# Performance work log

Hardware: AMD Instinct MI355X
Metric: run time of the kernel (lower is better)

Reference implementation:

```python
import jax, jax.numpy as jnp
import numpy as np

N_NODES = 100000
N_EDGES = 1600000
D_IN, D_HID, D_OUT = 64, 128, 64


def setup_inputs() -> dict:
    key = jax.random.key(0)
    ks = jax.random.split(key, 12)
    s = lambda d: 1.0 / np.sqrt(d)
    return {
        "x": jax.random.normal(ks[0], (N_NODES, D_IN), dtype=jnp.float32),
        "edge_index": jax.random.randint(ks[1], (2, N_EDGES), 0, N_NODES, dtype=jnp.int64),
        # conv1 MLP: Linear(D_IN->D_HID), ReLU, Linear(D_HID->D_HID)
        "W1a": jax.random.uniform(ks[2], (D_IN, D_HID), jnp.float32, -s(D_IN), s(D_IN)),
        "b1a": jnp.zeros((D_HID,), jnp.float32),
        "W1b": jax.random.uniform(ks[3], (D_HID, D_HID), jnp.float32, -s(D_HID), s(D_HID)),
        "b1b": jnp.zeros((D_HID,), jnp.float32),
        # conv2 MLP: Linear(D_HID->D_HID), ReLU, Linear(D_HID->D_HID)
        "W2a": jax.random.uniform(ks[4], (D_HID, D_HID), jnp.float32, -s(D_HID), s(D_HID)),
        "b2a": jnp.zeros((D_HID,), jnp.float32),
        "W2b": jax.random.uniform(ks[5], (D_HID, D_HID), jnp.float32, -s(D_HID), s(D_HID)),
        "b2b": jnp.zeros((D_HID,), jnp.float32),
        # final projection Linear(D_HID->D_OUT)
        "Wlin": jax.random.uniform(ks[6], (D_HID, D_OUT), jnp.float32, -s(D_HID), s(D_HID)),
        "blin": jnp.zeros((D_OUT,), jnp.float32),
    }


def _gin_conv(h, src, dst, Wa, ba, Wb, bb, num_nodes):
    # GINConv (eps=0): MLP((1+eps)*x + sum_{j->i} x_j)
    agg = jax.ops.segment_sum(h[src], dst, num_segments=num_nodes)  # [N, d]
    z = h + agg
    z = jax.nn.relu(z @ Wa + ba)
    return z @ Wb + bb


def reference(x, edge_index, W1a, b1a, W1b, b1b, W2a, b2a, W2b, b2b, Wlin, blin):
    n = x.shape[0]
    src, dst = edge_index[0], edge_index[1]
    h = jax.nn.relu(_gin_conv(x, src, dst, W1a, b1a, W1b, b1b, n))
    h = jax.nn.relu(_gin_conv(h, src, dst, W2a, b2a, W2b, b2b, n))
    return h @ Wlin + blin  # [N, D_OUT]
```

## Files before the change

kernel.cpp:

```cpp
#include <hip/hip_runtime.h>
#include <hip/hip_fp16.h>


typedef __attribute__((ext_vector_type(8))) short short8;
typedef __attribute__((ext_vector_type(4))) float f32x4;
union F8 { unsigned u[4]; short8 s; };

__device__ inline unsigned bfpair(float v) {
    unsigned u = __float_as_uint(v);
    unsigned rh = u + 0x7fffu + ((u >> 16) & 1u);
    unsigned hf = rh & 0xffff0000u;
    float lof = v - __uint_as_float(hf);
    unsigned ul = __float_as_uint(lof);
    unsigned rl = ul + 0x7fffu + ((ul >> 16) & 1u);
    return (rh >> 16) | (rl & 0xffff0000u);
}


constexpr int BUCKET_SHIFT = 9;
constexpr int BUCKET_NODES = 1 << BUCKET_SHIFT;
constexpr int CAP = 10240;
constexpr int EPB = 4096;
constexpr int NBUCK_MAX = 256;

__global__ __launch_bounds__(256) void bucket_scatter_kernel(const int* __restrict__ ei, int E,
                                                             int* __restrict__ gcur,
                                                             int* __restrict__ gpk,
                                                             int nbuck) {
    __shared__ int spk[EPB];
    __shared__ unsigned char sbuck[EPB];
    __shared__ int lcnt[NBUCK_MAX];
    __shared__ int lbase[NBUCK_MAX];
    __shared__ int lcur[NBUCK_MAX];
    __shared__ int gbase[NBUCK_MAX];
    __shared__ int stmp[256];

    const int t = threadIdx.x;
    const int e0 = blockIdx.x * EPB;
    const int ecnt = min(EPB, E - e0);

    for (int i = t; i < NBUCK_MAX; i += 256) lcnt[i] = 0;
    __syncthreads();

    for (int i = t; i < ecnt; i += 256) {
        int d = ei[E + e0 + i];
        atomicAdd(&lcnt[d >> BUCKET_SHIFT], 1);
    }
    __syncthreads();

    int v = lcnt[t];
    stmp[t] = v;
    __syncthreads();
    #pragma unroll
    for (int off = 1; off < 256; off <<= 1) {
        int add = (t >= off) ? stmp[t - off] : 0;
        __syncthreads();
        stmp[t] += add;
        __syncthreads();
    }
    lbase[t] = stmp[t] - v;
    lcur[t] = stmp[t] - v;
    __syncthreads();

    for (int i = t; i < ecnt; i += 256) {
        int s = ei[e0 + i];
        int d = ei[E + e0 + i];
        int b = d >> BUCKET_SHIFT;
        int p = atomicAdd(&lcur[b], 1);
        spk[p] = ((d & (BUCKET_NODES - 1)) << 17) | s;
        sbuck[p] = (unsigned char)b;
    }
    __syncthreads();

    if (t < nbuck) {
        int c = lcnt[t];
        gbase[t] = (c > 0) ? atomicAdd(&gcur[t], c) : 0;
    }
    __syncthreads();

    for (int i = t; i < ecnt; i += 256) {
        int b = sbuck[i];
        int gp = gbase[b] + (i - lbase[b]);
        if (gp < (b + 1) * CAP) gpk[gp] = spk[i];
    }
}

__global__ __launch_bounds__(256) void bucket_hist_kernel(const int* __restrict__ gpk,
                                                          const int* __restrict__ gcur,
                                                          int* __restrict__ cnt, int N) {
    __shared__ int h[BUCKET_NODES];
    const int t = threadIdx.x;
    const int b = blockIdx.x;
    const int base = b << BUCKET_SHIFT;
    for (int i = t; i < BUCKET_NODES; i += 256) h[i] = 0;
    __syncthreads();
    int cb = min(gcur[b] - b * CAP, CAP);
    const int* pp = gpk + (size_t)b * CAP;
    for (int i = t; i < cb; i += 256) atomicAdd(&h[((unsigned)pp[i]) >> 17], 1);
    __syncthreads();
    for (int i = t; i < BUCKET_NODES && base + i < N; i += 256) cnt[base + i] = h[i];
}

__global__ __launch_bounds__(256) void scan_block_kernel(const int* __restrict__ cnt,
                                                         int* __restrict__ rs,
                                                         int* __restrict__ partials,
                                                         int N) {
    __shared__ int s[256];
    int t = threadIdx.x;
    int i = blockIdx.x * 256 + t;
    int v = (i < N) ? cnt[i] : 0;
    s[t] = v;
    __syncthreads();
    #pragma unroll
    for (int off = 1; off < 256; off <<= 1) {
        int add = (t >= off) ? s[t - off] : 0;
        __syncthreads();
        s[t] += add;
        __syncthreads();
    }
    if (i < N) rs[i] = s[t] - v;
    if (t == 255) partials[blockIdx.x] = s[255];
}

__global__ __launch_bounds__(512) void scan_partials_kernel(int* __restrict__ partials,
                                                            int nb) {
    __shared__ int s[512];
    int t = threadIdx.x;
    int v = (t < nb) ? partials[t] : 0;
    s[t] = v;
    __syncthreads();
    #pragma unroll
    for (int off = 1; off < 512; off <<= 1) {
        int add = (t >= off) ? s[t - off] : 0;
        __syncthreads();
        s[t] += add;
        __syncthreads();
    }
    if (t < nb) partials[t] = s[t] - v;
}

__global__ __launch_bounds__(256) void scan_add_kernel(int* __restrict__ rs,
                                                       const int* __restrict__ partials,
                                                       int N, int E) {
    int i = blockIdx.x * 256 + threadIdx.x;
    if (i < N) rs[i] += partials[blockIdx.x];
    if (i == 0) rs[N] = E;
}

__global__ __launch_bounds__(256) void bucket_fill_kernel(const int* __restrict__ gpk,
                                                          const int* __restrict__ gcur,
                                                          const int* __restrict__ rs,
                                                          int* __restrict__ edge_src, int N) {
    __shared__ int cur[BUCKET_NODES];
    const int t = threadIdx.x;
    const int b = blockIdx.x;
    const int base = b << BUCKET_SHIFT;
    for (int i = t; i < BUCKET_NODES; i += 256) cur[i] = rs[min(base + i, N)];
    __syncthreads();
    int cb = min(gcur[b] - b * CAP, CAP);
    const int* pp = gpk + (size_t)b * CAP;
    for (int i = t; i < cb; i += 256) {
        unsigned pw = (unsigned)pp[i];
        int p = atomicAdd(&cur[pw >> 17], 1);
        edge_src[p] = (int)(pw & 0x1FFFFu);
    }
}


__global__ __launch_bounds__(256) void prep_kernel(const float* __restrict__ W1a,
                                                   const float* __restrict__ W1b,
                                                   const float* __restrict__ W2a,
                                                   const float* __restrict__ W2b,
                                                   const float* __restrict__ Wlin,
                                                   short* __restrict__ hi,
                                                   short* __restrict__ lo,
                                                   const float* __restrict__ x,
                                                   __half2* __restrict__ x16, int n2,
                                                   int* __restrict__ gcur, int nbuck) {
    int i = blockIdx.x * 256 + threadIdx.x;
    if (blockIdx.x == 0 && threadIdx.x < nbuck) gcur[threadIdx.x] = threadIdx.x * CAP;
    if (i < 65536) {
        const float* W;
        int base, K, N;
        if (i < 8192)       { W = W1a;  base = 0;     K = 64;  N = 128; }
        else if (i < 24576) { W = W1b;  base = 8192;  K = 128; N = 128; }
        else if (i < 40960) { W = W2a;  base = 24576; K = 128; N = 128; }
        else if (i < 57344) { W = W2b;  base = 40960; K = 128; N = 128; }
        else                { W = Wlin; base = 57344; K = 128; N = 64;  }
        int rel = i - base;
        int NT = N >> 4;
        int j  = rel & 7;
        int l  = (rel >> 3) & 63;
        int tc = rel >> 9;
        int nt = tc % NT;
        int c  = tc / NT;
        int n  = nt * 16 + (l & 15);
        int k  = c * 32 + ((l >> 4) << 3) + j;
        float v = W[k * N + n];
        unsigned p = bfpair(v);
        hi[i] = (short)(p & 0xffffu);
        lo[i] = (short)(p >> 16);
    }
    for (int k = i; k < n2; k += gridDim.x * 256) {
        float2 v = reinterpret_cast<const float2*>(x)[k];
        x16[k] = __floats2half2_rn(v.x, v.y);
    }
}


__device__ inline void acc8(float* a, const uint4& v) {
    const __half2* h = reinterpret_cast<const __half2*>(&v);
    #pragma unroll
    for (int j = 0; j < 4; ++j) {
        float2 f = __half22float2(h[j]);
        a[2 * j]     += f.x;
        a[2 * j + 1] += f.y;
    }
}

__device__ inline uint4 pack8(const float* a) {
    uint4 o;
    __half2 h;
    h = __floats2half2_rn(a[0], a[1]); o.x = *reinterpret_cast<unsigned*>(&h);
    h = __floats2half2_rn(a[2], a[3]); o.y = *reinterpret_cast<unsigned*>(&h);
    h = __floats2half2_rn(a[4], a[5]); o.z = *reinterpret_cast<unsigned*>(&h);
    h = __floats2half2_rn(a[6], a[7]); o.w = *reinterpret_cast<unsigned*>(&h);
    return o;
}

__global__ __launch_bounds__(256) void agg128_fp16(const __half2* __restrict__ H16,
                                                   const int* __restrict__ row_start,
                                                   const int* __restrict__ edge_src,
                                                   __half2* __restrict__ Z16, int N) {
    int wave = threadIdx.x >> 6, lane = threadIdx.x & 63;
    int node = blockIdx.x * 4 + wave;
    if (node >= N) return;
    const int lg = lane >> 4;
    const int lo = lane & 15;
    const uint4* Hv = reinterpret_cast<const uint4*>(H16);
    int beg = row_start[node], end = row_start[node + 1];

    uint4 selfv = Hv[(size_t)node * 16 + lo];

    float a[8];
    #pragma unroll
    for (int j = 0; j < 8; ++j) a[j] = 0.f;
    if (lg == 0) acc8(a, selfv);

    int i = beg;
    for (; i + 16 <= end; i += 16) {
        int s0 = edge_src[i + lg];
        int s1 = edge_src[i + 4 + lg];
        int s2 = edge_src[i + 8 + lg];
        int s3 = edge_src[i + 12 + lg];
        uint4 v0 = Hv[(size_t)s0 * 16 + lo];
        uint4 v1 = Hv[(size_t)s1 * 16 + lo];
        uint4 v2 = Hv[(size_t)s2 * 16 + lo];
        uint4 v3 = Hv[(size_t)s3 * 16 + lo];
        acc8(a, v0); acc8(a, v1); acc8(a, v2); acc8(a, v3);
    }
    if (i + 8 <= end) {
        int s0 = edge_src[i + lg];
        int s1 = edge_src[i + 4 + lg];
        uint4 v0 = Hv[(size_t)s0 * 16 + lo];
        uint4 v1 = Hv[(size_t)s1 * 16 + lo];
        acc8(a, v0); acc8(a, v1);
        i += 8;
    }
    if (i + 4 <= end) {
        int s0 = edge_src[i + lg];
        uint4 v0 = Hv[(size_t)s0 * 16 + lo];
        acc8(a, v0);
        i += 4;
    }
    int rem = end - i;
    if (lg < rem) {
        int s0 = edge_src[i + lg];
        uint4 v0 = Hv[(size_t)s0 * 16 + lo];
        acc8(a, v0);
    }

    #pragma unroll
    for (int j = 0; j < 8; ++j) {
        a[j] += __shfl_xor(a[j], 16);
        a[j] += __shfl_xor(a[j], 32);
    }

    if (lg == 0) {
        reinterpret_cast<uint4*>(Z16)[(size_t)node * 16 + lo] = pack8(a);
    }
}

__global__ __launch_bounds__(256) void agg64_fp16(const __half2* __restrict__ H16,
                                                  const int* __restrict__ row_start,
                                                  const int* __restrict__ edge_src,
                                                  __half2* __restrict__ Z16, int N) {
    int wave = threadIdx.x >> 6, lane = threadIdx.x & 63;
    int node = blockIdx.x * 4 + wave;
    if (node >= N) return;
    const int lg = lane >> 3;
    const int lo = lane & 7;
    const uint4* Hv = reinterpret_cast<const uint4*>(H16);
    int beg = row_start[node], end = row_start[node + 1];

    uint4 selfv = Hv[(size_t)node * 8 + lo];

    float a[8];
    #pragma unroll
    for (int j = 0; j < 8; ++j) a[j] = 0.f;
    if (lg == 0) acc8(a, selfv);

    int i = beg;
    for (; i + 16 <= end; i += 16) {
        int s0 = edge_src[i + lg];
        int s1 = edge_src[i + 8 + lg];
        uint4 v0 = Hv[(size_t)s0 * 8 + lo];
        uint4 v1 = Hv[(size_t)s1 * 8 + lo];
        acc8(a, v0); acc8(a, v1);
    }
    if (i + 8 <= end) {
        int s0 = edge_src[i + lg];
        uint4 v0 = Hv[(size_t)s0 * 8 + lo];
        acc8(a, v0);
        i += 8;
    }
    int rem = end - i;
    if (lg < rem) {
        int s0 = edge_src[i + lg];
        uint4 v0 = Hv[(size_t)s0 * 8 + lo];
        acc8(a, v0);
    }

    #pragma unroll
    for (int j = 0; j < 8; ++j) {
        a[j] += __shfl_xor(a[j], 8);
        a[j] += __shfl_xor(a[j], 16);
        a[j] += __shfl_xor(a[j], 32);
    }

    if (lg == 0) {
        reinterpret_cast<uint4*>(Z16)[(size_t)node * 8 + lo] = pack8(a);
    }
}


template <int K>
__device__ inline void stage_global16(const __half2* __restrict__ z, int M, int m0,
                                      unsigned* __restrict__ P, int t) {
    constexpr int KC = K / 32;
    constexpr int NF = 8 * KC * 64;
    #pragma unroll
    for (int fi = t; fi < NF; fi += 256) {
        int l = fi & 63;
        int tc = fi >> 6;
        int c = tc & (KC - 1);
        int T = tc / KC;
        int row = m0 + T * 16 + (l & 15);
        if (row >= M) row = M - 1;
        int kb = c * 32 + ((l >> 4) << 3);
        const __half2* p = z + (size_t)row * (K / 2) + (kb >> 1);
        uint4 v = *reinterpret_cast<const uint4*>(p);
        float2 f0 = __half22float2(*reinterpret_cast<__half2*>(&v.x));
        float2 f1 = __half22float2(*reinterpret_cast<__half2*>(&v.y));
        float2 f2 = __half22float2(*reinterpret_cast<__half2*>(&v.z));
        float2 f3 = __half22float2(*reinterpret_cast<__half2*>(&v.w));
        int base = ((T * KC + c) * 8) * 66 + l;
        P[base + 0 * 66] = bfpair(f0.x);
        P[base + 1 * 66] = bfpair(f0.y);
        P[base + 2 * 66] = bfpair(f1.x);
        P[base + 3 * 66] = bfpair(f1.y);
        P[base + 4 * 66] = bfpair(f2.x);
        P[base + 5 * 66] = bfpair(f2.y);
        P[base + 6 * 66] = bfpair(f3.x);
        P[base + 7 * 66] = bfpair(f3.y);
    }
}

template <int K, int NT>
__device__ inline void stage_compute(const unsigned* __restrict__ P,
                                     const short* __restrict__ WH,
                                     const short* __restrict__ WL,
                                     int w, int lane, f32x4 (*acc)[8]) {
    constexpr int KC = K / 32;
    const short8* bhp = reinterpret_cast<const short8*>(WH) + lane;
    const short8* blp = reinterpret_cast<const short8*>(WL) + lane;
    for (int c = 0; c < KC; ++c) {
        F8 bh[NT], bl[NT];
        #pragma unroll
        for (int nt = 0; nt < NT; ++nt) {
            bh[nt].s = bhp[(c * NT + nt) * 64];
            bl[nt].s = blp[(c * NT + nt) * 64];
        }
        #pragma unroll
        for (int mt = 0; mt < 2; ++mt) {
            const int T = w * 2 + mt;
            const unsigned* Pb = P + ((T * KC + c) * 8) * 66 + lane;
            unsigned d[8];
            #pragma unroll
            for (int j = 0; j < 8; ++j) d[j] = Pb[j * 66];
            F8 ah, al;
            #pragma unroll
            for (int j = 0; j < 4; ++j) {
                ah.u[j] = __builtin_amdgcn_perm(d[2 * j + 1], d[2 * j], 0x05040100u);
                al.u[j] = __builtin_amdgcn_perm(d[2 * j + 1], d[2 * j], 0x07060302u);
            }
            #pragma unroll
            for (int nt = 0; nt < NT; ++nt) {
                acc[mt][nt] = __builtin_amdgcn_mfma_f32_16x16x32_bf16(ah.s, bh[nt].s, acc[mt][nt], 0, 0, 0);
                acc[mt][nt] = __builtin_amdgcn_mfma_f32_16x16x32_bf16(al.s, bh[nt].s, acc[mt][nt], 0, 0, 0);
                acc[mt][nt] = __builtin_amdgcn_mfma_f32_16x16x32_bf16(ah.s, bl[nt].s, acc[mt][nt], 0, 0, 0);
            }
        }
    }
}

__device__ inline void epilogue_tile(const f32x4* acc, const float* __restrict__ bias,
                                     unsigned* __restrict__ Pout, int T, int lane) {
    int q = lane >> 4, ln = lane & 15;
    #pragma unroll
    for (int nt = 0; nt < 8; ++nt) {
        int col = nt * 16 + ln;
        float b = bias[col];
        int c = col >> 5, jj = col & 7, q2 = (col >> 3) & 3;
        int pb = ((T * 4 + c) * 8 + jj) * 66;
        #pragma unroll
        for (int r = 0; r < 4; ++r) {
            float v = fmaxf(acc[nt][r] + b, 0.f);
            Pout[pb + ((q * 4 + r) | (q2 << 4))] = bfpair(v);
        }
    }
}

__global__ __launch_bounds__(256, 2) void mfma_mlp_A(const __half2* __restrict__ z16,
                                                     const short* __restrict__ WaH,
                                                     const short* __restrict__ WaL,
                                                     const float* __restrict__ ba,
                                                     const short* __restrict__ WbH,
                                                     const short* __restrict__ WbL,
                                                     const float* __restrict__ bb,
                                                     __half* __restrict__ H16out, int M) {
    __shared__ unsigned P[8 * 4 * 8 * 66];
    const int t = threadIdx.x;
    const int w = t >> 6, lane = t & 63;
    const int m0 = blockIdx.x * 128;
    const int q = lane >> 4, ln = lane & 15;

    stage_global16<64>(z16, M, m0, P, t);
    __syncthreads();

    f32x4 acc[2][8];
    #pragma unroll
    for (int mt = 0; mt < 2; ++mt)
        #pragma unroll
        for (int i = 0; i < 8; ++i) acc[mt][i] = (f32x4){0.f, 0.f, 0.f, 0.f};
    stage_compute<64, 8>(P, WaH, WaL, w, lane, acc);
    __syncthreads();
    epilogue_tile(acc[0], ba, P, w * 2 + 0, lane);
    epilogue_tile(acc[1], ba, P, w * 2 + 1, lane);
    __syncthreads();

    #pragma unroll
    for (int mt = 0; mt < 2; ++mt)
        #pragma unroll
        for (int i = 0; i < 8; ++i) acc[mt][i] = (f32x4){0.f, 0.f, 0.f, 0.f};
    stage_compute<128, 8>(P, WbH, WbL, w, lane, acc);

    #pragma unroll
    for (int mt = 0; mt < 2; ++mt) {
        #pragma unroll
        for (int nt = 0; nt < 8; ++nt) {
            int col = nt * 16 + ln;
            float b = bb[col];
            #pragma unroll
            for (int r = 0; r < 4; ++r) {
                int row = m0 + (w * 2 + mt) * 16 + q * 4 + r;
                if (row < M) {
                    float v = fmaxf(acc[mt][nt][r] + b, 0.f);
                    H16out[(size_t)row * 128 + col] = __float2half_rn(v);
                }
            }
        }
    }
}

__global__ __launch_bounds__(256, 2) void mfma_mlp_B(const __half2* __restrict__ z16,
                                                     const short* __restrict__ WaH,
                                                     const short* __restrict__ WaL,
                                                     const float* __restrict__ ba,
                                                     const short* __restrict__ WbH,
                                                     const short* __restrict__ WbL,
                                                     const float* __restrict__ bb,
                                                     const short* __restrict__ WlH,
                                                     const short* __restrict__ WlL,
                                                     const float* __restrict__ bl,
                                                     float* __restrict__ Out, int M) {
    __shared__ unsigned P[8 * 4 * 8 * 66];
    const int t = threadIdx.x;
    const int w = t >> 6, lane = t & 63;
    const int m0 = blockIdx.x * 128;
    const int q = lane >> 4, ln = lane & 15;

    stage_global16<128>(z16, M, m0, P, t);
    __syncthreads();

    f32x4 acc[2][8];
    #pragma unroll
    for (int mt = 0; mt < 2; ++mt)
        #pragma unroll
        for (int i = 0; i < 8; ++i) acc[mt][i] = (f32x4){0.f, 0.f, 0.f, 0.f};
    stage_compute<128, 8>(P, WaH, WaL, w, lane, acc);
    __syncthreads();
    epilogue_tile(acc[0], ba, P, w * 2 + 0, lane);
    epilogue_tile(acc[1], ba, P, w * 2 + 1, lane);
    __syncthreads();

    #pragma unroll
    for (int mt = 0; mt < 2; ++mt)
        #pragma unroll
        for (int i = 0; i < 8; ++i) acc[mt][i] = (f32x4){0.f, 0.f, 0.f, 0.f};
    stage_compute<128, 8>(P, WbH, WbL, w, lane, acc);
    __syncthreads();
    epilogue_tile(acc[0], bb, P, w * 2 + 0, lane);
    epilogue_tile(acc[1], bb, P, w * 2 + 1, lane);
    __syncthreads();

    #pragma unroll
    for (int mt = 0; mt < 2; ++mt)
        #pragma unroll
        for (int i = 0; i < 8; ++i) acc[mt][i] = (f32x4){0.f, 0.f, 0.f, 0.f};
    stage_compute<128, 4>(P, WlH, WlL, w, lane, acc);

    #pragma unroll
    for (int mt = 0; mt < 2; ++mt) {
        #pragma unroll
        for (int nt = 0; nt < 4; ++nt) {
            int col = nt * 16 + ln;
            float b = bl[col];
            #pragma unroll
            for (int r = 0; r < 4; ++r) {
                int row = m0 + (w * 2 + mt) * 16 + q * 4 + r;
                if (row < M) Out[(size_t)row * 64 + col] = acc[mt][nt][r] + b;
            }
        }
    }
}


extern "C" void kernel_launch(void* const* d_in, const int* in_sizes, int n_in,
                              void* d_out, int out_size, void* d_ws, size_t ws_size,
                              hipStream_t stream) {
    const float* x    = (const float*)d_in[0];
    const int*   ei   = (const int*)d_in[1];
    const float* W1a  = (const float*)d_in[2];
    const float* b1a  = (const float*)d_in[3];
    const float* W1b  = (const float*)d_in[4];
    const float* b1b  = (const float*)d_in[5];
    const float* W2a  = (const float*)d_in[6];
    const float* b2a  = (const float*)d_in[7];
    const float* W2b  = (const float*)d_in[8];
    const float* b2b  = (const float*)d_in[9];
    const float* Wlin = (const float*)d_in[10];
    const float* blin = (const float*)d_in[11];
    float* out = (float*)d_out;

    const int N = in_sizes[0] / 64;
    const int E = in_sizes[1] / 2;
    const int NBUCK = (N + BUCKET_NODES - 1) >> BUCKET_SHIFT;

    char* ws = (char*)d_ws;
    const size_t bufBytes = (size_t)N * 128 * sizeof(float);
    __half2* Zbuf = (__half2*)(ws + 0);
    char* B = ws + bufBytes;
    size_t off = 3 * bufBytes;
    int* row_start = (int*)(ws + off); off += ((size_t)(N + 1) * 4 + 15) & ~(size_t)15;
    int* cnt       = (int*)(ws + off); off += ((size_t)N * 4 + 15) & ~(size_t)15;
    int* partials  = (int*)(ws + off); off += 4096;
    int* gcur      = (int*)(ws + off); off += 4096;
    int* edge_src  = (int*)(ws + off); off += (size_t)E * 4;
    __half* h116   = (__half*)(ws + off); off += (size_t)N * 128 * 2;
    int* gpk = (int*)B;
    short* wHi = (short*)(B + (32u << 20));
    short* wLo = wHi + 65536;
    __half* x16 = (__half*)(B + (36u << 20));
    short* w1aH = wHi + 0;     short* w1aL = wLo + 0;
    short* w1bH = wHi + 8192;  short* w1bL = wLo + 8192;
    short* w2aH = wHi + 24576; short* w2aL = wLo + 24576;
    short* w2bH = wHi + 40960; short* w2bL = wLo + 40960;
    short* wlH  = wHi + 57344; short* wlL  = wLo + 57344;

    const int NB_N = (N + 255) / 256;
    const int NB_G = (N + 127) / 128;
    const int NB_S = (E + EPB - 1) / EPB;
    const int NB_A128 = (N + 3) / 4;
    const int NB_A64  = (N + 3) / 4;
    const int NB_P = 12500;

    prep_kernel<<<NB_P, 256, 0, stream>>>(W1a, W1b, W2a, W2b, Wlin, wHi, wLo,
                                          x, (__half2*)x16, N * 32, gcur, NBUCK);

    bucket_scatter_kernel<<<NB_S, 256, 0, stream>>>(ei, E, gcur, gpk, NBUCK);
    bucket_hist_kernel<<<NBUCK, 256, 0, stream>>>(gpk, gcur, cnt, N);
    scan_block_kernel<<<NB_N, 256, 0, stream>>>(cnt, row_start, partials, N);
    scan_partials_kernel<<<1, 512, 0, stream>>>(partials, NB_N);
    scan_add_kernel<<<NB_N, 256, 0, stream>>>(row_start, partials, N, E);
    bucket_fill_kernel<<<NBUCK, 256, 0, stream>>>(gpk, gcur, row_start, edge_src, N);

    agg64_fp16<<<NB_A64, 256, 0, stream>>>((const __half2*)x16, row_start, edge_src, Zbuf, N);
    mfma_mlp_A<<<NB_G, 256, 0, stream>>>(Zbuf, w1aH, w1aL, b1a, w1bH, w1bL, b1b, h116, N);

    agg128_fp16<<<NB_A128, 256, 0, stream>>>((const __half2*)h116, row_start, edge_src, Zbuf, N);
    mfma_mlp_B<<<NB_G, 256, 0, stream>>>(Zbuf, w2aH, w2aL, b2a, w2bH, w2bL, b2b,
                                         wlH, wlL, blin, out, N);
}
```

Before: 355.5 us.

## Fuse CSR histogram, scan and fill into per-bucket build kernel

```diff
diff --git a/kernel.cpp b/kernel.cpp
--- a/kernel.cpp
+++ b/kernel.cpp
@@ -85,31 +85,15 @@
     }
 }
 
-__global__ __launch_bounds__(256) void bucket_hist_kernel(const int* __restrict__ gpk,
-                                                          const int* __restrict__ gcur,
-                                                          int* __restrict__ cnt, int N) {
-    __shared__ int h[BUCKET_NODES];
-    const int t = threadIdx.x;
-    const int b = blockIdx.x;
-    const int base = b << BUCKET_SHIFT;
-    for (int i = t; i < BUCKET_NODES; i += 256) h[i] = 0;
-    __syncthreads();
-    int cb = min(gcur[b] - b * CAP, CAP);
-    const int* pp = gpk + (size_t)b * CAP;
-    for (int i = t; i < cb; i += 256) atomicAdd(&h[((unsigned)pp[i]) >> 17], 1);
-    __syncthreads();
-    for (int i = t; i < BUCKET_NODES && base + i < N; i += 256) cnt[base + i] = h[i];
-}
-
-__global__ __launch_bounds__(256) void scan_block_kernel(const int* __restrict__ cnt,
-                                                         int* __restrict__ rs,
-                                                         int* __restrict__ partials,
-                                                         int N) {
+__global__ __launch_bounds__(256) void bucket_base_kernel(const int* __restrict__ gcur,
+                                                          int* __restrict__ bbase,
+                                                          int* __restrict__ row_start,
+                                                          int nbuck, int N, int E) {
     __shared__ int s[256];
     int t = threadIdx.x;
-    int i = blockIdx.x * 256 + t;
-    int v = (i < N) ? cnt[i] : 0;
-    s[t] = v;
+    int c = 0;
+    if (t < nbuck) c = min(gcur[t] - t * CAP, CAP);
+    s[t] = c;
     __syncthreads();
     #pragma unroll
     for (int off = 1; off < 256; off <<= 1) {
@@ -118,50 +102,51 @@
         s[t] += add;
         __syncthreads();
     }
-    if (i < N) rs[i] = s[t] - v;
-    if (t == 255) partials[blockIdx.x] = s[255];
-}
-
-__global__ __launch_bounds__(512) void scan_partials_kernel(int* __restrict__ partials,
-                                                            int nb) {
-    __shared__ int s[512];
-    int t = threadIdx.x;
-    int v = (t < nb) ? partials[t] : 0;
-    s[t] = v;
-    __syncthreads();
-    #pragma unroll
-    for (int off = 1; off < 512; off <<= 1) {
+    if (t < nbuck) bbase[t] = s[t] - c;
+    if (t == 0) row_start[N] = E;
+}
+
+__global__ __launch_bounds__(256) void bucket_build_kernel(const int* __restrict__ gpk,
+                                                           const int* __restrict__ gcur,
+                                                           const int* __restrict__ bbase,
+                                                           int* __restrict__ row_start,
+                                                           int* __restrict__ edge_src, int N) {
+    __shared__ int h[BUCKET_NODES];
+    __shared__ int s[256];
+    const int t = threadIdx.x;
+    const int b = blockIdx.x;
+    const int base = b << BUCKET_SHIFT;
+
+    for (int i = t; i < BUCKET_NODES; i += 256) h[i] = 0;
+    __syncthreads();
+
+    int cb = min(gcur[b] - b * CAP, CAP);
+    const int* pp = gpk + (size_t)b * CAP;
+    for (int i = t; i < cb; i += 256) atomicAdd(&h[((unsigned)pp[i]) >> 17], 1);
+    __syncthreads();
+
+    int c0 = h[2 * t], c1 = h[2 * t + 1];
+    int psum = c0 + c1;
+    s[t] = psum;
+    __syncthreads();
+    #pragma unroll
+    for (int off = 1; off < 256; off <<= 1) {
         int add = (t >= off) ? s[t - off] : 0;
         __syncthreads();
         s[t] += add;
         __syncthreads();
     }
-    if (t < nb) partials[t] = s[t] - v;
-}
-
-__global__ __launch_bounds__(256) void scan_add_kernel(int* __restrict__ rs,
-                                                       const int* __restrict__ partials,
-                                                       int N, int E) {
-    int i = blockIdx.x * 256 + threadIdx.x;
-    if (i < N) rs[i] += partials[blockIdx.x];
-    if (i == 0) rs[N] = E;
-}
-
-__global__ __launch_bounds__(256) void bucket_fill_kernel(const int* __restrict__ gpk,
-                                                          const int* __restrict__ gcur,
-                                                          const int* __restrict__ rs,
-                                                          int* __restrict__ edge_src, int N) {
-    __shared__ int cur[BUCKET_NODES];
-    const int t = threadIdx.x;
-    const int b = blockIdx.x;
-    const int base = b << BUCKET_SHIFT;
-    for (int i = t; i < BUCKET_NODES; i += 256) cur[i] = rs[min(base + i, N)];
-    __syncthreads();
-    int cb = min(gcur[b] - b * CAP, CAP);
-    const int* pp = gpk + (size_t)b * CAP;
+    int ex = s[t] - psum + bbase[b];
+    __syncthreads();
+    h[2 * t]     = ex;
+    h[2 * t + 1] = ex + c0;
+    if (base + 2 * t < N)     row_start[base + 2 * t]     = ex;
+    if (base + 2 * t + 1 < N) row_start[base + 2 * t + 1] = ex + c0;
+    __syncthreads();
+
     for (int i = t; i < cb; i += 256) {
         unsigned pw = (unsigned)pp[i];
-        int p = atomicAdd(&cur[pw >> 17], 1);
+        int p = atomicAdd(&h[pw >> 17], 1);
         edge_src[p] = (int)(pw & 0x1FFFFu);
     }
 }
@@ -587,8 +572,8 @@
     short* w2aH = wHi + 24576; short* w2aL = wLo + 24576;
     short* w2bH = wHi + 40960; short* w2bL = wLo + 40960;
     short* wlH  = wHi + 57344; short* wlL  = wLo + 57344;
-
-    const int NB_N = (N + 255) / 256;
+    (void)cnt;
+
     const int NB_G = (N + 127) / 128;
     const int NB_S = (E + EPB - 1) / EPB;
     const int NB_A128 = (N + 3) / 4;
@@ -599,11 +584,9 @@
                                           x, (__half2*)x16, N * 32, gcur, NBUCK);
 
     bucket_scatter_kernel<<<NB_S, 256, 0, stream>>>(ei, E, gcur, gpk, NBUCK);
-    bucket_hist_kernel<<<NBUCK, 256, 0, stream>>>(gpk, gcur, cnt, N);
-    scan_block_kernel<<<NB_N, 256, 0, stream>>>(cnt, row_start, partials, N);
-    scan_partials_kernel<<<1, 512, 0, stream>>>(partials, NB_N);
-    scan_add_kernel<<<NB_N, 256, 0, stream>>>(row_start, partials, N, E);
-    bucket_fill_kernel<<<NBUCK, 256, 0, stream>>>(gpk, gcur, row_start, edge_src, N);
+    bucket_base_kernel<<<1, 256, 0, stream>>>(gcur, partials, row_start, NBUCK, N, E);
+    bucket_build_kernel<<<NBUCK, 256, 0, stream>>>(gpk, gcur, partials, row_start,
+                                                   edge_src, N);
 
     agg64_fp16<<<NB_A64, 256, 0, stream>>>((const __half2*)x16, row_start, edge_src, Zbuf, N);
     mfma_mlp_A<<<NB_G, 256, 0, stream>>>(Zbuf, w1aH, w1aL, b1a, w1bH, w1bL, b1b, h116, N);
```

After: 352.0 us. No clear change (-1.0%).
